# Performance work log

Measured on AMD Instinct MI355X. Metric: run time of the kernel, lower is better.

Reference implementation:

```python
import jax, jax.numpy as jnp
import numpy as np

N_USERS = 100000
N_ENTITYS = 1000000
K_DIM = 64
T_DIM = 64
B = 2048
DEG = 32
N0 = B * DEG  # hop-0 frontier size


def setup_inputs() -> dict:
    key = jax.random.key(0)
    ks = jax.random.split(key, 11)
    return {
        "entity_emb": jax.random.normal(ks[0], (N_ENTITYS, K_DIM), jnp.float32) * 0.1,
        "user_emb": jax.random.normal(ks[1], (N_USERS, K_DIM), jnp.float32) * 0.1,
        "Wa": jax.random.normal(ks[2], (K_DIM, T_DIM), jnp.float32) * 0.05,
        "ba": jnp.zeros((T_DIM,), jnp.float32),
        "Wh": jax.random.normal(ks[3], (T_DIM, 1), jnp.float32) * 0.05,
        "bh": jnp.zeros((1,), jnp.float32),
        "u": jax.random.randint(ks[4], (B,), 0, N_USERS),
        "item_ids": jax.random.randint(ks[5], (B,), 0, N_ENTITYS),
        "nbr1_idx": jax.random.randint(ks[6], (B, DEG), 0, N0),
        "node_ids0": jax.random.randint(ks[7], (N0,), 0, N_ENTITYS),
        "nbr0": jax.random.randint(ks[8], (N0, DEG), 0, N_ENTITYS),
    }


def _lookup(table, idx):
    # nn.Embedding(max_norm=1): renormalize accessed rows to norm <= 1 (renorm
    # itself is done without grad in torch, hence stop_gradient on the scale).
    e = table[idx]
    n = jnp.sqrt(jnp.sum(e * e, axis=-1, keepdims=True))
    scale = jax.lax.stop_gradient(jnp.minimum(1.0, 1.0 / jnp.maximum(n, 1e-12)))
    return e * scale


def _fm(x):
    # FM sum-square trick over the neighbor axis (dim=1).
    s = jnp.sum(x, axis=1)
    return s * s - jnp.sum(x * x, axis=1)


def _attention(embs, Wa, ba, Wh, bh):
    h = jax.nn.relu(embs @ Wa + ba)      # [N, t]
    s = h @ Wh + bh                      # [N, 1]
    return jax.nn.softmax(s, axis=1)     # softmax over singleton dim (== ones), faithful to source


def reference(entity_emb, user_emb, Wa, ba, Wh, bh, u, item_ids, nbr1_idx, node_ids0, nbr0):
    # ---- hop 0 ----
    ent0 = _lookup(entity_emb, nbr0)        # [N0, deg, k]
    tgt0 = _lookup(entity_emb, node_ids0)   # [N0, k]
    agg0 = _fm(ent0)                        # [N0, k]
    att0 = _attention(tgt0 * agg0, Wa, ba, Wh, bh)  # atten_way == 'item'
    agg0 = att0 * agg0 + tgt0               # [N0, k]
    # ---- hop 1: regather hop-0 aggregates by neighbor index ----
    ent1 = agg0[nbr1_idx]                   # [B, deg, k]
    tgt1 = _lookup(entity_emb, item_ids)    # [B, k]
    agg1 = _fm(ent1)                        # [B, k]
    att1 = _attention(tgt1 * agg1, Wa, ba, Wh, bh)
    items = att1 * agg1 + tgt1              # [B, k]
    # ---- user-item score ----
    users = _lookup(user_emb, u)            # [B, k]
    logit = jax.nn.sigmoid(jnp.sum(users * items, axis=1))  # [B]
    return logit
```

## Files before the change

kernel.cpp:

```cpp
#include <hip/hip_runtime.h>
#include <math.h>

#define K_DIM 64
#define DEG 32

__device__ __forceinline__ float wave_sum(float v) {
    #pragma unroll
    for (int off = 32; off > 0; off >>= 1)
        v += __shfl_xor(v, off, 64);
    return v;
}

__device__ __forceinline__ float group16_sum(float v) {
    int x;
    x = __builtin_amdgcn_update_dpp(0, __float_as_int(v), 0x121, 0xf, 0xf, true);
    v += __int_as_float(x);
    x = __builtin_amdgcn_update_dpp(0, __float_as_int(v), 0x122, 0xf, 0xf, true);
    v += __int_as_float(x);
    x = __builtin_amdgcn_update_dpp(0, __float_as_int(v), 0x124, 0xf, 0xf, true);
    v += __int_as_float(x);
    x = __builtin_amdgcn_update_dpp(0, __float_as_int(v), 0x128, 0xf, 0xf, true);
    v += __int_as_float(x);
    return v;
}

__device__ __forceinline__ float renorm_scale(float n2) {
    return fminf(1.0f, __frsqrt_rn(n2));
}

__global__ void gafm_bitmap_zero(unsigned int* __restrict__ bitmap, int n_words) {
    int i = blockIdx.x * blockDim.x + threadIdx.x;
    if (i < n_words) bitmap[i] = 0u;
}

__global__ void gafm_bitmap_mark(const int* __restrict__ nbr1_idx,
                                 unsigned int* __restrict__ bitmap, int n) {
    int i = blockIdx.x * blockDim.x + threadIdx.x;
    if (i < n) {
        int j = nbr1_idx[i];
        atomicOr(&bitmap[j >> 5], 1u << (j & 31));
    }
}

__global__ __launch_bounds__(256) void gafm_hop0(
    const float4* __restrict__ emb4,
    const int*    __restrict__ node_ids0,
    const int*    __restrict__ nbr0,
    const unsigned int* __restrict__ bitmap,
    float4*       __restrict__ agg0_4,
    int n0)
{
    const int lane = threadIdx.x & 63;
    const int wave_in_blk = threadIdx.x >> 6;
    const int c   = lane & 15;
    const int g16 = lane & 48;
    const int row = blockIdx.x * 16 + wave_in_blk * 4 + (lane >> 4);
    if (row >= n0) return;
    if (bitmap && !((bitmap[row >> 5] >> (row & 31)) & 1u)) return;

    const int2 my_idx = ((const int2*)(nbr0 + (size_t)row * DEG))[c];

    float Sx = 0.f, Sy = 0.f, Sz = 0.f, Sw = 0.f;
    float Qx = 0.f, Qy = 0.f, Qz = 0.f, Qw = 0.f;

    #pragma unroll
    for (int b = 0; b < DEG / 8; ++b) {
        float4 buf[8];
        #pragma unroll
        for (int t = 0; t < 8; ++t) {
            const int d = b * 8 + t;
            const int src = g16 | (d >> 1);
            const int idx = __shfl((d & 1) ? my_idx.y : my_idx.x, src, 64);
            buf[t] = emb4[(size_t)idx * 16 + c];
        }
        #pragma unroll
        for (int t = 0; t < 8; ++t) {
            float4 v = buf[t];
            float n2 = fmaf(v.x, v.x, fmaf(v.y, v.y, fmaf(v.z, v.z, v.w * v.w)));
            n2 = group16_sum(n2);
            float r = renorm_scale(n2);
            float ex = v.x * r, ey = v.y * r, ez = v.z * r, ew = v.w * r;
            Sx += ex; Sy += ey; Sz += ez; Sw += ew;
            Qx = fmaf(ex, ex, Qx); Qy = fmaf(ey, ey, Qy);
            Qz = fmaf(ez, ez, Qz); Qw = fmaf(ew, ew, Qw);
        }
    }

    int tidx = node_ids0[row];
    float4 t = emb4[(size_t)tidx * 16 + c];
    float tn2 = fmaf(t.x, t.x, fmaf(t.y, t.y, fmaf(t.z, t.z, t.w * t.w)));
    tn2 = group16_sum(tn2);
    float tr = renorm_scale(tn2);

    float4 o;
    o.x = fmaf(Sx, Sx, -Qx) + t.x * tr;
    o.y = fmaf(Sy, Sy, -Qy) + t.y * tr;
    o.z = fmaf(Sz, Sz, -Qz) + t.z * tr;
    o.w = fmaf(Sw, Sw, -Qw) + t.w * tr;
    agg0_4[(size_t)row * 16 + c] = o;
}

__global__ __launch_bounds__(256) void gafm_hop1(
    const float* __restrict__ entity_emb,
    const float* __restrict__ user_emb,
    const int*   __restrict__ u_ids,
    const int*   __restrict__ item_ids,
    const int*   __restrict__ nbr1_idx,
    const float* __restrict__ agg0,
    float*       __restrict__ out,
    int nb_rows)
{
    int wave = (int)((blockIdx.x * blockDim.x + threadIdx.x) >> 6);
    int lane = threadIdx.x & 63;
    if (wave >= nb_rows) return;

    const int* nb = nbr1_idx + (size_t)wave * DEG;
    float S = 0.0f, Q = 0.0f;
    #pragma unroll 8
    for (int d = 0; d < DEG; ++d) {
        int j = nb[d];
        float e = agg0[(size_t)j * K_DIM + lane];
        S += e;
        Q = fmaf(e, e, Q);
    }
    float agg1 = fmaf(S, S, -Q);

    int ti = item_ids[wave];
    float t = entity_emb[(size_t)ti * K_DIM + lane];
    t *= renorm_scale(wave_sum(t * t));
    float items = agg1 + t;

    int ui = u_ids[wave];
    float uu = user_emb[(size_t)ui * K_DIM + lane];
    uu *= renorm_scale(wave_sum(uu * uu));

    float dot = wave_sum(uu * items);
    if (lane == 0)
        out[wave] = 1.0f / (1.0f + expf(-dot));
}

extern "C" void kernel_launch(void* const* d_in, const int* in_sizes, int n_in,
                              void* d_out, int out_size, void* d_ws, size_t ws_size,
                              hipStream_t stream) {
    const float* entity_emb = (const float*)d_in[0];
    const float* user_emb   = (const float*)d_in[1];
    const int*   u_ids      = (const int*)d_in[6];
    const int*   item_ids   = (const int*)d_in[7];
    const int*   nbr1_idx   = (const int*)d_in[8];
    const int*   node_ids0  = (const int*)d_in[9];
    const int*   nbr0       = (const int*)d_in[10];
    float*       out        = (float*)d_out;

    const int B      = in_sizes[6];
    const int N0     = in_sizes[9];
    const int NB1    = in_sizes[8];

    float* agg0 = (float*)d_ws;
    const size_t agg0_bytes = (size_t)N0 * K_DIM * sizeof(float);
    const int n_words = (N0 + 31) / 32;

    unsigned int* bitmap = nullptr;
    if (ws_size >= agg0_bytes + (size_t)n_words * 4) {
        bitmap = (unsigned int*)((char*)d_ws + agg0_bytes);
        gafm_bitmap_zero<<<(n_words + 255) / 256, 256, 0, stream>>>(bitmap, n_words);
        gafm_bitmap_mark<<<(NB1 + 255) / 256, 256, 0, stream>>>(nbr1_idx, bitmap, NB1);
    }

    int blocks0 = (N0 + 15) / 16;
    gafm_hop0<<<blocks0, 256, 0, stream>>>((const float4*)entity_emb, node_ids0,
                                           nbr0, bitmap, (float4*)agg0, N0);

    int blocks1 = (B + 3) / 4;
    gafm_hop1<<<blocks1, 256, 0, stream>>>(entity_emb, user_emb, u_ids, item_ids,
                                           nbr1_idx, agg0, out, B);
}
```

Baseline: 76.18 us.

## Compact live hop-0 rows into a dense list before the gather kernel

Adds a ballot/atomic stream-compaction kernel that turns the neighbor bitmap into a packed list of hop-0 rows that are actually referenced. Hop-0 then launches threads over that list, so its waves no longer sit mostly idle after bitmap early-exits, and row work is packed densely. The cost is one extra kernel launch plus an atomic counter. The workspace-size guard is gone and the bitmap path is now unconditional, so a too-small workspace would overflow.

Result: slower. 91.11 us (+19.6%).

```diff
diff --git a/kernel.cpp b/kernel.cpp
--- a/kernel.cpp
+++ b/kernel.cpp
@@ -28,9 +28,11 @@
     return fminf(1.0f, __frsqrt_rn(n2));
 }
 
-__global__ void gafm_bitmap_zero(unsigned int* __restrict__ bitmap, int n_words) {
+__global__ void gafm_bitmap_zero(unsigned int* __restrict__ bitmap, int n_words,
+                                 int* __restrict__ live_count) {
     int i = blockIdx.x * blockDim.x + threadIdx.x;
     if (i < n_words) bitmap[i] = 0u;
+    if (i == 0) *live_count = 0;
 }
 
 __global__ void gafm_bitmap_mark(const int* __restrict__ nbr1_idx,
@@ -42,21 +44,37 @@
     }
 }
 
+__global__ void gafm_compact(const unsigned int* __restrict__ bitmap,
+                             int* __restrict__ live_rows,
+                             int* __restrict__ live_count, int n0) {
+    int i = blockIdx.x * blockDim.x + threadIdx.x;
+    int lane = threadIdx.x & 63;
+    bool live = (i < n0) && ((bitmap[i >> 5] >> (i & 31)) & 1u);
+    unsigned long long mask = __ballot(live);
+    int base = 0;
+    if (lane == 0 && mask) base = atomicAdd(live_count, __popcll(mask));
+    base = __shfl(base, 0, 64);
+    if (live) {
+        int pre = __popcll(mask & ((1ull << lane) - 1ull));
+        live_rows[base + pre] = i;
+    }
+}
+
 __global__ __launch_bounds__(256) void gafm_hop0(
     const float4* __restrict__ emb4,
     const int*    __restrict__ node_ids0,
     const int*    __restrict__ nbr0,
-    const unsigned int* __restrict__ bitmap,
-    float4*       __restrict__ agg0_4,
-    int n0)
+    const int*    __restrict__ live_rows,
+    const int*    __restrict__ live_count,
+    float4*       __restrict__ agg0_4)
 {
     const int lane = threadIdx.x & 63;
     const int wave_in_blk = threadIdx.x >> 6;
     const int c   = lane & 15;
     const int g16 = lane & 48;
-    const int row = blockIdx.x * 16 + wave_in_blk * 4 + (lane >> 4);
-    if (row >= n0) return;
-    if (bitmap && !((bitmap[row >> 5] >> (row & 31)) & 1u)) return;
+    const int g   = blockIdx.x * 16 + wave_in_blk * 4 + (lane >> 4);
+    if (g >= *live_count) return;
+    const int row = live_rows[g];
 
     const int2 my_idx = ((const int2*)(nbr0 + (size_t)row * DEG))[c];
 
@@ -151,24 +169,25 @@
     const int*   nbr0       = (const int*)d_in[10];
     float*       out        = (float*)d_out;
 
-    const int B      = in_sizes[6];
-    const int N0     = in_sizes[9];
-    const int NB1    = in_sizes[8];
+    const int B   = in_sizes[6];
+    const int N0  = in_sizes[9];
+    const int NB1 = in_sizes[8];
 
     float* agg0 = (float*)d_ws;
     const size_t agg0_bytes = (size_t)N0 * K_DIM * sizeof(float);
     const int n_words = (N0 + 31) / 32;
+    unsigned int* bitmap   = (unsigned int*)((char*)d_ws + agg0_bytes);
+    int* live_count        = (int*)(bitmap + n_words);
+    int* live_rows         = live_count + 1;
 
-    unsigned int* bitmap = nullptr;
-    if (ws_size >= agg0_bytes + (size_t)n_words * 4) {
-        bitmap = (unsigned int*)((char*)d_ws + agg0_bytes);
-        gafm_bitmap_zero<<<(n_words + 255) / 256, 256, 0, stream>>>(bitmap, n_words);
-        gafm_bitmap_mark<<<(NB1 + 255) / 256, 256, 0, stream>>>(nbr1_idx, bitmap, NB1);
-    }
+    gafm_bitmap_zero<<<(n_words + 255) / 256, 256, 0, stream>>>(bitmap, n_words, live_count);
+    gafm_bitmap_mark<<<(NB1 + 255) / 256, 256, 0, stream>>>(nbr1_idx, bitmap, NB1);
+    gafm_compact<<<(N0 + 255) / 256, 256, 0, stream>>>(bitmap, live_rows, live_count, N0);
 
     int blocks0 = (N0 + 15) / 16;
     gafm_hop0<<<blocks0, 256, 0, stream>>>((const float4*)entity_emb, node_ids0,
-                                           nbr0, bitmap, (float4*)agg0, N0);
+                                           nbr0, live_rows, live_count,
+                                           (float4*)agg0);
 
     int blocks1 = (B + 3) / 4;
     gafm_hop1<<<blocks1, 256, 0, stream>>>(entity_emb, user_emb, u_ids, item_ids,
```
